# Kernel tuning notes

Measured on AMD Instinct MI355X. Metric: run time of the kernel, lower is better.

## Reference

```python
import jax, jax.numpy as jnp
import numpy as np

N, F, H = 512, 256, 512

def _w(k, i, o):
    return jax.random.normal(k, (i, o), jnp.float32) * (1.0 / np.sqrt(i))

def setup_inputs() -> dict:
    key = jax.random.key(0)
    ks = jax.random.split(key, 12)
    z = lambda n: jnp.zeros((n,), jnp.float32)
    return {
        "node_features": jax.random.normal(ks[0], (N, F), jnp.float32),
        "adjacency": jax.random.uniform(ks[1], (N, N), jnp.float32),
        # GraphConv layers: neighbor linear (wl,bl) and self-loop (ws,bs)
        "gc1_wl": _w(ks[2], F, H), "gc1_bl": z(H), "gc1_ws": _w(ks[3], F, H), "gc1_bs": z(H),
        "gc2_wl": _w(ks[4], H, H), "gc2_bl": z(H), "gc2_ws": _w(ks[5], H, H), "gc2_bs": z(H),
        "gc3_wl": _w(ks[6], H, F), "gc3_bl": z(F), "gc3_ws": _w(ks[7], H, F), "gc3_bs": z(F),
        # edge MLP: Linear(2F,H) -> ReLU -> (dropout=identity, eval) -> Linear(H,H) -> ReLU -> Linear(H,1)
        "mlp_w1": _w(ks[8], 2 * F, H), "mlp_b1": z(H),
        "mlp_w2": _w(ks[9], H, H), "mlp_b2": z(H),
        "mlp_w3": _w(ks[10], H, 1), "mlp_b3": z(1),
    }

def _gconv(x, adj_norm, wl, bl, ws, bs):
    # adj_norm @ Linear(x) + SelfLoop(x)
    return adj_norm @ (x @ wl + bl) + (x @ ws + bs)

def reference(node_features, adjacency,
              gc1_wl, gc1_bl, gc1_ws, gc1_bs,
              gc2_wl, gc2_bl, gc2_ws, gc2_bs,
              gc3_wl, gc3_bl, gc3_ws, gc3_bs,
              mlp_w1, mlp_b1, mlp_w2, mlp_b2, mlp_w3, mlp_b3):
    # row-normalized adjacency (shared across all three layers)
    adj_norm = adjacency / (adjacency.sum(axis=1, keepdims=True) + 1e-8)
    x = jax.nn.relu(_gconv(node_features, adj_norm, gc1_wl, gc1_bl, gc1_ws, gc1_bs))
    x = jax.nn.relu(_gconv(x, adj_norm, gc2_wl, gc2_bl, gc2_ws, gc2_bs))
    emb = _gconv(x, adj_norm, gc3_wl, gc3_bl, gc3_ws, gc3_bs)  # [N, F]
    # vectorized all-pairs (i<j) edge scoring, symmetric scatter
    iu, ju = np.triu_indices(N, k=1)  # static index lists, P = N(N-1)/2
    ef = jnp.concatenate([emb[iu], emb[ju]], axis=-1)  # [P, 2F]
    h = jax.nn.relu(ef @ mlp_w1 + mlp_b1)
    h = jax.nn.relu(h @ mlp_w2 + mlp_b2)
    s = jax.nn.sigmoid((h @ mlp_w3 + mlp_b3)[:, 0])  # [P]
    edge_scores = jnp.zeros((N, N), emb.dtype).at[iu, ju].set(s).at[ju, iu].set(s)
    return emb, edge_scores
```

## Files before the change

### kernel.cpp

```cpp
#include <hip/hip_runtime.h>
#include <hip/hip_bf16.h>


#define NN 512
#define FF 256
#define HH 512

typedef __attribute__((ext_vector_type(8))) short s8v;
typedef __attribute__((ext_vector_type(4))) float f4v;

__device__ __forceinline__ ushort f2bf(float f) {
  unsigned u = __float_as_uint(f);
  unsigned r = (u + 0x7fffu + ((u >> 16) & 1u)) >> 16;
  return (ushort)r;
}

template <bool RELU>
__device__ __forceinline__ void gemm_tile64(
    int m0, int n0, int K,
    const float* __restrict__ A, int lda,
    const float* __restrict__ B, int ldb,
    const float* __restrict__ bias,
    const float* __restrict__ add, int ldadd,
    float* __restrict__ C, int ldc, int tid)
{
  __shared__ float As[64][18];
  __shared__ float Bs[64][68];
  float4 acc = {0.f, 0.f, 0.f, 0.f};
  const int ty = tid >> 4, tx = tid & 15;

  const int am = tid >> 4;
  const int ak = tid & 15;
  const int bk = tid >> 4;
  const int bn = tid & 15;

  float4 pa = *(const float4*)&A[(m0 + am) * lda + ak * 4];
  float4 pb0 = *(const float4*)&B[bk * ldb + n0 + bn * 4];
  float4 pb1 = *(const float4*)&B[(bk + 16) * ldb + n0 + bn * 4];
  float4 pb2 = *(const float4*)&B[(bk + 32) * ldb + n0 + bn * 4];
  float4 pb3 = *(const float4*)&B[(bk + 48) * ldb + n0 + bn * 4];

  for (int k0 = 0; k0 < K; k0 += 64) {
    As[ak * 4 + 0][am] = pa.x;
    As[ak * 4 + 1][am] = pa.y;
    As[ak * 4 + 2][am] = pa.z;
    As[ak * 4 + 3][am] = pa.w;
    *(float4*)&Bs[bk][bn * 4] = pb0;
    *(float4*)&Bs[bk + 16][bn * 4] = pb1;
    *(float4*)&Bs[bk + 32][bn * 4] = pb2;
    *(float4*)&Bs[bk + 48][bn * 4] = pb3;
    __syncthreads();
    if (k0 + 64 < K) {
      pa = *(const float4*)&A[(m0 + am) * lda + k0 + 64 + ak * 4];
      pb0 = *(const float4*)&B[(k0 + 64 + bk) * ldb + n0 + bn * 4];
      pb1 = *(const float4*)&B[(k0 + 80 + bk) * ldb + n0 + bn * 4];
      pb2 = *(const float4*)&B[(k0 + 96 + bk) * ldb + n0 + bn * 4];
      pb3 = *(const float4*)&B[(k0 + 112 + bk) * ldb + n0 + bn * 4];
    }
#pragma unroll
    for (int k = 0; k < 64; ++k) {
      float a = As[k][ty];
      float4 b = *(const float4*)&Bs[k][tx * 4];
      acc.x += a * b.x; acc.y += a * b.y; acc.z += a * b.z; acc.w += a * b.w;
    }
    __syncthreads();
  }

  int m = m0 + ty;
  float4 v = acc;
  if (bias) {
    float4 bv = *(const float4*)&bias[n0 + tx * 4];
    v.x += bv.x; v.y += bv.y; v.z += bv.z; v.w += bv.w;
  }
  if (add) {
    float4 d = *(const float4*)&add[m * ldadd + n0 + tx * 4];
    v.x += d.x; v.y += d.y; v.z += d.z; v.w += d.w;
  }
  if (RELU) {
    v.x = fmaxf(v.x, 0.f); v.y = fmaxf(v.y, 0.f);
    v.z = fmaxf(v.z, 0.f); v.w = fmaxf(v.w, 0.f);
  }
  *(float4*)&C[m * ldc + n0 + tx * 4] = v;
}

template <bool RELU>
__global__ __launch_bounds__(512)
void gemm_ks(int K,
             const float* __restrict__ A, int lda,
             const float* __restrict__ B0, const float* __restrict__ B1, int ldb,
             const float* __restrict__ bias0, const float* __restrict__ bias1,
             const float* __restrict__ add0, const float* __restrict__ add1, int ldadd,
             float* __restrict__ C0, float* __restrict__ C1, int ldc)
{
  const float* B = blockIdx.z ? B1 : B0;
  const float* bias = blockIdx.z ? bias1 : bias0;
  const float* add = blockIdx.z ? add1 : add0;
  float* C = blockIdx.z ? C1 : C0;
  const int n0 = blockIdx.x * 64;
  const int m0 = blockIdx.y * 16;
  const int tid = threadIdx.x;
  const int half = tid >> 8;
  const int t = tid & 255;
  const int ty = t >> 4, tx = t & 15;

  __shared__ float As[2][64][18];
  __shared__ float Bs[2][64][68];
  __shared__ float red[16][68];

  float4 acc = {0.f, 0.f, 0.f, 0.f};
  const int am = t >> 4, ak = t & 15;
  const int bk = t >> 4, bn = t & 15;
  const int Kh = K >> 1;
  const int kb = half * Kh;

  float4 pa = *(const float4*)&A[(m0 + am) * lda + kb + ak * 4];
  float4 pb0 = *(const float4*)&B[(kb + bk) * ldb + n0 + bn * 4];
  float4 pb1 = *(const float4*)&B[(kb + bk + 16) * ldb + n0 + bn * 4];
  float4 pb2 = *(const float4*)&B[(kb + bk + 32) * ldb + n0 + bn * 4];
  float4 pb3 = *(const float4*)&B[(kb + bk + 48) * ldb + n0 + bn * 4];

  for (int k0 = 0; k0 < Kh; k0 += 64) {
    As[half][ak * 4 + 0][am] = pa.x;
    As[half][ak * 4 + 1][am] = pa.y;
    As[half][ak * 4 + 2][am] = pa.z;
    As[half][ak * 4 + 3][am] = pa.w;
    *(float4*)&Bs[half][bk][bn * 4] = pb0;
    *(float4*)&Bs[half][bk + 16][bn * 4] = pb1;
    *(float4*)&Bs[half][bk + 32][bn * 4] = pb2;
    *(float4*)&Bs[half][bk + 48][bn * 4] = pb3;
    __syncthreads();
    if (k0 + 64 < Kh) {
      pa = *(const float4*)&A[(m0 + am) * lda + kb + k0 + 64 + ak * 4];
      pb0 = *(const float4*)&B[(kb + k0 + 64 + bk) * ldb + n0 + bn * 4];
      pb1 = *(const float4*)&B[(kb + k0 + 80 + bk) * ldb + n0 + bn * 4];
      pb2 = *(const float4*)&B[(kb + k0 + 96 + bk) * ldb + n0 + bn * 4];
      pb3 = *(const float4*)&B[(kb + k0 + 112 + bk) * ldb + n0 + bn * 4];
    }
#pragma unroll
    for (int k = 0; k < 64; ++k) {
      float a = As[half][k][ty];
      float4 b = *(const float4*)&Bs[half][k][tx * 4];
      acc.x += a * b.x; acc.y += a * b.y; acc.z += a * b.z; acc.w += a * b.w;
    }
    __syncthreads();
  }

  if (half) *(float4*)&red[ty][tx * 4] = acc;
  __syncthreads();
  if (!half) {
    float4 r = *(const float4*)&red[ty][tx * 4];
    float4 v = acc;
    v.x += r.x; v.y += r.y; v.z += r.z; v.w += r.w;
    int m = m0 + ty;
    if (bias) {
      float4 bv = *(const float4*)&bias[n0 + tx * 4];
      v.x += bv.x; v.y += bv.y; v.z += bv.z; v.w += bv.w;
    }
    if (add) {
      float4 d = *(const float4*)&add[m * ldadd + n0 + tx * 4];
      v.x += d.x; v.y += d.y; v.z += d.z; v.w += d.w;
    }
    if (RELU) {
      v.x = fmaxf(v.x, 0.f); v.y = fmaxf(v.y, 0.f);
      v.z = fmaxf(v.z, 0.f); v.w = fmaxf(v.w, 0.f);
    }
    *(float4*)&C[m * ldc + n0 + tx * 4] = v;
  }
}

template <bool RELU>
__global__ __launch_bounds__(1024)
void gemm_ks4(int K,
              const float* __restrict__ A, int lda,
              const float* __restrict__ B0, const float* __restrict__ B1, int ldb,
              const float* __restrict__ bias0, const float* __restrict__ bias1,
              const float* __restrict__ add0, const float* __restrict__ add1, int ldadd,
              float* __restrict__ C0, float* __restrict__ C1, int ldc)
{
  const float* B = blockIdx.z ? B1 : B0;
  const float* bias = blockIdx.z ? bias1 : bias0;
  const float* add = blockIdx.z ? add1 : add0;
  float* C = blockIdx.z ? C1 : C0;
  const int n0 = blockIdx.x * 64;
  const int m0 = blockIdx.y * 16;
  const int tid = threadIdx.x;
  const int q = tid >> 8;
  const int t = tid & 255;
  const int ty = t >> 4, tx = t & 15;

  __shared__ float As[4][64][18];
  __shared__ float Bs[4][64][68];
  __shared__ float red[3][16][68];

  float4 acc = {0.f, 0.f, 0.f, 0.f};
  const int am = ty, ak = tx;
  const int bk = ty, bn = tx;
  const int Kq = K >> 2;
  const int kb = q * Kq;

  float4 pa = *(const float4*)&A[(m0 + am) * lda + kb + ak * 4];
  float4 pb0 = *(const float4*)&B[(kb + bk) * ldb + n0 + bn * 4];
  float4 pb1 = *(const float4*)&B[(kb + bk + 16) * ldb + n0 + bn * 4];
  float4 pb2 = *(const float4*)&B[(kb + bk + 32) * ldb + n0 + bn * 4];
  float4 pb3 = *(const float4*)&B[(kb + bk + 48) * ldb + n0 + bn * 4];

  for (int k0 = 0; k0 < Kq; k0 += 64) {
    As[q][ak * 4 + 0][am] = pa.x;
    As[q][ak * 4 + 1][am] = pa.y;
    As[q][ak * 4 + 2][am] = pa.z;
    As[q][ak * 4 + 3][am] = pa.w;
    *(float4*)&Bs[q][bk][bn * 4] = pb0;
    *(float4*)&Bs[q][bk + 16][bn * 4] = pb1;
    *(float4*)&Bs[q][bk + 32][bn * 4] = pb2;
    *(float4*)&Bs[q][bk + 48][bn * 4] = pb3;
    __syncthreads();
    if (k0 + 64 < Kq) {
      pa = *(const float4*)&A[(m0 + am) * lda + kb + k0 + 64 + ak * 4];
      pb0 = *(const float4*)&B[(kb + k0 + 64 + bk) * ldb + n0 + bn * 4];
      pb1 = *(const float4*)&B[(kb + k0 + 80 + bk) * ldb + n0 + bn * 4];
      pb2 = *(const float4*)&B[(kb + k0 + 96 + bk) * ldb + n0 + bn * 4];
      pb3 = *(const float4*)&B[(kb + k0 + 112 + bk) * ldb + n0 + bn * 4];
    }
#pragma unroll
    for (int k = 0; k < 64; ++k) {
      float a = As[q][k][ty];
      float4 b = *(const float4*)&Bs[q][k][tx * 4];
      acc.x += a * b.x; acc.y += a * b.y; acc.z += a * b.z; acc.w += a * b.w;
    }
    __syncthreads();
  }

  if (q) *(float4*)&red[q - 1][ty][tx * 4] = acc;
  __syncthreads();
  if (!q) {
    float4 v = acc;
#pragma unroll
    for (int r = 0; r < 3; ++r) {
      float4 p = *(const float4*)&red[r][ty][tx * 4];
      v.x += p.x; v.y += p.y; v.z += p.z; v.w += p.w;
    }
    int m = m0 + ty;
    if (bias) {
      float4 bv = *(const float4*)&bias[n0 + tx * 4];
      v.x += bv.x; v.y += bv.y; v.z += bv.z; v.w += bv.w;
    }
    if (add) {
      float4 d = *(const float4*)&add[m * ldadd + n0 + tx * 4];
      v.x += d.x; v.y += d.y; v.z += d.z; v.w += d.w;
    }
    if (RELU) {
      v.x = fmaxf(v.x, 0.f); v.y = fmaxf(v.y, 0.f);
      v.z = fmaxf(v.z, 0.f); v.w = fmaxf(v.w, 0.f);
    }
    *(float4*)&C[m * ldc + n0 + tx * 4] = v;
  }
}

__global__ __launch_bounds__(256)
void prep_gemm1(const float* __restrict__ adj, float* __restrict__ adjn,
                const float* __restrict__ w2, ushort* __restrict__ w2t2,
                const float* __restrict__ node,
                const float* __restrict__ g1wl, const float* __restrict__ g1bl,
                const float* __restrict__ g1ws, const float* __restrict__ g1bs,
                float* __restrict__ Tb, float* __restrict__ Sb) {
  int b = blockIdx.x;
  int tid = threadIdx.x;
  if (b < 512) {
    int z = b >> 8, t = b & 255;
    int m0 = (t >> 3) * 16, n0 = (t & 7) * 64;
    gemm_tile64<false>(m0, n0, FF, node, FF, z ? g1ws : g1wl, HH,
                       z ? g1bs : g1bl, nullptr, 0, z ? Sb : Tb, HH, tid);
  } else if (b < 1024) {
    int row = b - 512;
    const float* r = adj + row * NN;
    float a0 = r[tid], a1 = r[tid + 256];
    float s = a0 + a1;
#pragma unroll
    for (int m = 1; m < 64; m <<= 1) s += __shfl_xor(s, m);
    __shared__ float wsum[4];
    if ((tid & 63) == 0) wsum[tid >> 6] = s;
    __syncthreads();
    float inv = 1.f / (wsum[0] + wsum[1] + wsum[2] + wsum[3] + 1e-8f);
    float* o = adjn + row * NN;
    o[tid] = a0 * inv;
    o[tid + 256] = a1 * inv;
  } else {
    int b2 = b - 1024;
    int slab = b2 >> 3;
    int col = (b2 & 7) * 64 + (tid >> 2);
    int kq = tid & 3;
    int k0 = slab * 32 + kq * 8;
    ushort tmp[8];
#pragma unroll
    for (int e = 0; e < 8; ++e) tmp[e] = f2bf(w2[(k0 + e) * HH + col]);
    ushort* dst = w2t2 + slab * 16384 + col * 32 + kq * 8;
    *(ushort4*)dst = *(ushort4*)tmp;
    *(ushort4*)(dst + 4) = *(ushort4*)&tmp[4];
  }
}

__global__ __launch_bounds__(512)
__attribute__((amdgpu_waves_per_eu(2, 2)))
void edge_mlp(const float* __restrict__ Amat, const float* __restrict__ Bmat,
              const ushort* __restrict__ w2t2,
              const float* __restrict__ b2, const float* __restrict__ w3,
              const float* __restrict__ b3,
              float* __restrict__ edges)
{
  __shared__ ushort h1s[2][128 * 128];
  __shared__ float rowsv[2][24][128];
  __shared__ float part[8][128];

  const int tb = (int)blockIdx.x;
  int bj = (int)((sqrtf(4.f * tb + 1.f) - 1.f) * 0.5f);
  while (bj * bj + bj > tb) --bj;
  while ((bj + 1) * (bj + 2) <= tb) ++bj;
  const int bi = tb - bj * bj - bj;

  const int tid = threadIdx.x;
  const int wid = tid >> 6;
  const int lane = tid & 63;
  const int l15 = lane & 15;
  const int lg = lane >> 4;

  const f4v zero = {0.f, 0.f, 0.f, 0.f};
  f4v acc[8][4];
#pragma unroll
  for (int mf = 0; mf < 8; ++mf)
#pragma unroll
    for (int nf = 0; nf < 4; ++nf) acc[mf][nf] = zero;

  const int r1 = tid >> 5, kc1 = tid & 31;
  const int r2 = 16 + (tid >> 5);
  const float* src1base = (r1 < 8) ? (Amat + (bi * 8 + r1) * HH)
                                   : (Bmat + (bj * 16 + r1 - 8) * HH);
  const float* src2base = Bmat + (bj * 16 + r2 - 8) * HH;

  float4 ra, rb;
  auto issue_rows = [&](int ch) {
    ra = *(const float4*)(src1base + ch * 128 + kc1 * 4);
    if (tid < 256) rb = *(const float4*)(src2base + ch * 128 + kc1 * 4);
  };
  auto write_rows = [&](int buf) {
    *(float4*)&rowsv[buf][r1][kc1 * 4] = ra;
    if (tid < 256) *(float4*)&rowsv[buf][r2][kc1 * 4] = rb;
  };
  auto build_h1 = [&](int buf) {
#pragma unroll
    for (int q = 0; q < 8; ++q) {
      int fidx = q * 512 + tid;
      int p = fidx >> 5;
      int k4 = fidx & 31;
      float4 av = *(const float4*)&rowsv[buf][p >> 4][k4 * 4];
      float4 bv = *(const float4*)&rowsv[buf][8 + (p & 15)][k4 * 4];
      ushort4 pk;
      pk.x = f2bf(fmaxf(av.x + bv.x, 0.f));
      pk.y = f2bf(fmaxf(av.y + bv.y, 0.f));
      pk.z = f2bf(fmaxf(av.z + bv.z, 0.f));
      pk.w = f2bf(fmaxf(av.w + bv.w, 0.f));
      int off = (p * 256 + k4 * 8) ^ ((p & 7) << 4);
      *(ushort4*)((char*)h1s[buf] + off) = pk;
    }
  };

  auto lgkm_barrier = [] {
    asm volatile("s_waitcnt lgkmcnt(0)" ::: "memory");
    __builtin_amdgcn_s_barrier();
  };

  issue_rows(0);
  write_rows(0);
  lgkm_barrier();
  build_h1(0);
  lgkm_barrier();

  const ushort* wbase = w2t2 + wid * 2048 + l15 * 32 + lg * 8;

  s8v nb0, nb1, nb2, nb3;
  nb0 = *(const s8v*)wbase;
  nb1 = *(const s8v*)(wbase + 512);
  nb2 = *(const s8v*)(wbase + 1024);
  nb3 = *(const s8v*)(wbase + 1536);

  auto slab_step = [&](int cur, int slab) {
    s8v cb0 = nb0, cb1 = nb1, cb2 = nb2, cb3 = nb3;
    if (slab < 15) {
      const ushort* wb = wbase + (slab + 1) * 16384;
      nb0 = *(const s8v*)wb;
      nb1 = *(const s8v*)(wb + 512);
      nb2 = *(const s8v*)(wb + 1024);
      nb3 = *(const s8v*)(wb + 1536);
    }
    int ks = slab & 3;
    __builtin_amdgcn_s_setprio(1);
#pragma unroll
    for (int mf = 0; mf < 8; ++mf) {
      int p = mf * 16 + l15;
      int off = (p * 256 + ks * 64 + lg * 16) ^ ((p & 7) << 4);
      s8v a = *(const s8v*)((const char*)h1s[cur] + off);
      acc[mf][0] = __builtin_amdgcn_mfma_f32_16x16x32_bf16(a, cb0, acc[mf][0], 0, 0, 0);
      acc[mf][1] = __builtin_amdgcn_mfma_f32_16x16x32_bf16(a, cb1, acc[mf][1], 0, 0, 0);
      acc[mf][2] = __builtin_amdgcn_mfma_f32_16x16x32_bf16(a, cb2, acc[mf][2], 0, 0, 0);
      acc[mf][3] = __builtin_amdgcn_mfma_f32_16x16x32_bf16(a, cb3, acc[mf][3], 0, 0, 0);
    }
    __builtin_amdgcn_s_setprio(0);
  };

#pragma unroll
  for (int ch = 0; ch < 4; ++ch) {
    int cur = ch & 1;
    if (ch < 3) issue_rows(ch + 1);
    slab_step(cur, ch * 4 + 0);
    slab_step(cur, ch * 4 + 1);
    if (ch < 3) write_rows(cur ^ 1);
    slab_step(cur, ch * 4 + 2);
    if (ch < 3) lgkm_barrier();
    slab_step(cur, ch * 4 + 3);
    if (ch < 3) {
      build_h1(cur ^ 1);
      lgkm_barrier();
    }
  }

  float bb[4], ww[4];
#pragma unroll
  for (int nf = 0; nf < 4; ++nf) {
    int col = wid * 64 + nf * 16 + l15;
    bb[nf] = b2[col];
    ww[nf] = w3[col];
  }
#pragma unroll
  for (int mf = 0; mf < 8; ++mf) {
    float ps[4];
#pragma unroll
    for (int e = 0; e < 4; ++e) {
      ps[e] = fmaxf(acc[mf][0][e] + bb[0], 0.f) * ww[0] +
              fmaxf(acc[mf][1][e] + bb[1], 0.f) * ww[1] +
              fmaxf(acc[mf][2][e] + bb[2], 0.f) * ww[2] +
              fmaxf(acc[mf][3][e] + bb[3], 0.f) * ww[3];
    }
#pragma unroll
    for (int m = 1; m < 16; m <<= 1) {
#pragma unroll
      for (int e = 0; e < 4; ++e) ps[e] += __shfl_xor(ps[e], m);
    }
    if (l15 == 0) {
#pragma unroll
      for (int e = 0; e < 4; ++e)
        part[wid][mf * 16 + lg * 4 + e] = ps[e];
    }
  }
  __syncthreads();
  if (tid < 128) {
    float tot = b3[0];
#pragma unroll
    for (int w = 0; w < 8; ++w) tot += part[w][tid];
    float sg = 1.f / (1.f + expf(-tot));
    int i = bi * 8 + (tid >> 4);
    int j = bj * 16 + (tid & 15);
    if (i < j) {
      edges[i * NN + j] = sg;
      edges[j * NN + i] = sg;
    } else if (i == j) {
      edges[i * NN + i] = 0.f;
    }
  }
}

extern "C" void kernel_launch(void* const* d_in, const int* in_sizes, int n_in,
                              void* d_out, int out_size, void* d_ws, size_t ws_size,
                              hipStream_t stream) {
  const float* node = (const float*)d_in[0];
  const float* adj  = (const float*)d_in[1];
  const float* g1wl = (const float*)d_in[2];
  const float* g1bl = (const float*)d_in[3];
  const float* g1ws = (const float*)d_in[4];
  const float* g1bs = (const float*)d_in[5];
  const float* g2wl = (const float*)d_in[6];
  const float* g2bl = (const float*)d_in[7];
  const float* g2ws = (const float*)d_in[8];
  const float* g2bs = (const float*)d_in[9];
  const float* g3wl = (const float*)d_in[10];
  const float* g3bl = (const float*)d_in[11];
  const float* g3ws = (const float*)d_in[12];
  const float* g3bs = (const float*)d_in[13];
  const float* w1 = (const float*)d_in[14];
  const float* b1 = (const float*)d_in[15];
  const float* w2 = (const float*)d_in[16];
  const float* b2 = (const float*)d_in[17];
  const float* w3 = (const float*)d_in[18];
  const float* b3 = (const float*)d_in[19];

  float* out = (float*)d_out;
  float* emb = out;
  float* edges = out + NN * FF;

  char* wsb = (char*)d_ws;
  float* adjn = (float*)wsb;
  float* Tb   = (float*)(wsb + (1u << 20));
  float* Sb   = (float*)(wsb + (2u << 20));
  float* xa   = (float*)(wsb + (3u << 20));
  float* xb   = (float*)(wsb + (4u << 20));
  ushort* w2t2 = (ushort*)(wsb + (5u << 20));
  float* Amat = Tb;
  float* Bmat = Sb;

  prep_gemm1<<<1152, 256, 0, stream>>>(adj, adjn, w2, w2t2, node,
                                       g1wl, g1bl, g1ws, g1bs, Tb, Sb);
  gemm_ks4<true><<<dim3(8, 32, 1), 1024, 0, stream>>>(
      NN, adjn, NN, Tb, Tb, HH, nullptr, nullptr,
      Sb, Sb, HH, xa, xa, HH);
  gemm_ks<false><<<dim3(8, 32, 2), 512, 0, stream>>>(
      HH, xa, HH, g2wl, g2ws, HH, g2bl, g2bs,
      nullptr, nullptr, 0, Tb, Sb, HH);
  gemm_ks4<true><<<dim3(8, 32, 1), 1024, 0, stream>>>(
      NN, adjn, NN, Tb, Tb, HH, nullptr, nullptr,
      Sb, Sb, HH, xb, xb, HH);
  gemm_ks4<false><<<dim3(4, 32, 2), 1024, 0, stream>>>(
      HH, xb, HH, g3wl, g3ws, FF, g3bl, g3bs,
      nullptr, nullptr, 0, Tb, Sb, FF);
  gemm_ks4<false><<<dim3(4, 32, 1), 1024, 0, stream>>>(
      NN, adjn, NN, Tb, Tb, FF, nullptr, nullptr,
      Sb, Sb, FF, emb, emb, FF);
  gemm_ks<false><<<dim3(8, 32, 2), 512, 0, stream>>>(
      FF, emb, FF, w1, w1 + FF * HH, HH, b1, nullptr,
      nullptr, nullptr, 0, Amat, Bmat, HH);

  edge_mlp<<<1056, 512, 0, stream>>>(Amat, Bmat, w2t2, b2, w3, b3, edges);
}
```

Baseline: 166.7 us.

## Reassociate layer-3 and first MLP linear via precomposed weights, cutting a dependent GEMM

Layer 3 is restructured as V3 = adjn @ xb, then emb and the MLP's first-layer projections Amat/Bmat are all computed directly from [V3, xb] against precomposed weight products (g3wl@w1 etc.) built in the prep kernel. This removes one serial GEMM from the dependency chain and merges the remaining ones into a single concatenated-K launch. The cost is extra weight-product GEMMs in prep, a bias-fold loop, more workspace, and changed fp32 rounding order. The path is gated on workspace size.

```diff
diff --git a/kernel.cpp b/kernel.cpp
--- a/kernel.cpp
+++ b/kernel.cpp
@@ -256,13 +256,100 @@
   }
 }
 
+__global__ __launch_bounds__(512)
+void gemm_cat(const float* __restrict__ V3, const float* __restrict__ xb,
+              const float* __restrict__ g3wl, const float* __restrict__ g3ws,
+              const float* __restrict__ CwA1, const float* __restrict__ CwA2,
+              const float* __restrict__ CwB1, const float* __restrict__ CwB2,
+              const float* __restrict__ g3b, const float* __restrict__ biasA,
+              const float* __restrict__ biasB,
+              float* __restrict__ emb, float* __restrict__ Amat,
+              float* __restrict__ Bmat)
+{
+  const int z = blockIdx.z;
+  if (z == 0 && blockIdx.x >= 4) return;
+  const float* B1; const float* B2; const float* bias; float* C;
+  int ldb, ldc;
+  if (z == 0)      { B1 = g3wl; B2 = g3ws; bias = g3b;   C = emb;  ldb = 256; ldc = 256; }
+  else if (z == 1) { B1 = CwA1; B2 = CwA2; bias = biasA; C = Amat; ldb = 512; ldc = 512; }
+  else             { B1 = CwB1; B2 = CwB2; bias = biasB; C = Bmat; ldb = 512; ldc = 512; }
+
+  const int n0 = blockIdx.x * 64;
+  const int m0 = blockIdx.y * 16;
+  const int tid = threadIdx.x;
+  const int half = tid >> 8;
+  const int t = tid & 255;
+  const int ty = t >> 4, tx = t & 15;
+  const float* A = half ? xb : V3;
+  const float* B = half ? B2 : B1;
+
+  __shared__ float As[2][64][18];
+  __shared__ float Bs[2][64][68];
+  __shared__ float red[16][68];
+
+  float4 acc = {0.f, 0.f, 0.f, 0.f};
+  const int am = ty, ak = tx;
+  const int bk = ty, bn = tx;
+
+  float4 pa = *(const float4*)&A[(m0 + am) * 512 + ak * 4];
+  float4 pb0 = *(const float4*)&B[bk * ldb + n0 + bn * 4];
+  float4 pb1 = *(const float4*)&B[(bk + 16) * ldb + n0 + bn * 4];
+  float4 pb2 = *(const float4*)&B[(bk + 32) * ldb + n0 + bn * 4];
+  float4 pb3 = *(const float4*)&B[(bk + 48) * ldb + n0 + bn * 4];
+
+  for (int k0 = 0; k0 < 512; k0 += 64) {
+    As[half][ak * 4 + 0][am] = pa.x;
+    As[half][ak * 4 + 1][am] = pa.y;
+    As[half][ak * 4 + 2][am] = pa.z;
+    As[half][ak * 4 + 3][am] = pa.w;
+    *(float4*)&Bs[half][bk][bn * 4] = pb0;
+    *(float4*)&Bs[half][bk + 16][bn * 4] = pb1;
+    *(float4*)&Bs[half][bk + 32][bn * 4] = pb2;
+    *(float4*)&Bs[half][bk + 48][bn * 4] = pb3;
+    __syncthreads();
+    if (k0 + 64 < 512) {
+      pa = *(const float4*)&A[(m0 + am) * 512 + k0 + 64 + ak * 4];
+      pb0 = *(const float4*)&B[(k0 + 64 + bk) * ldb + n0 + bn * 4];
+      pb1 = *(const float4*)&B[(k0 + 80 + bk) * ldb + n0 + bn * 4];
+      pb2 = *(const float4*)&B[(k0 + 96 + bk) * ldb + n0 + bn * 4];
+      pb3 = *(const float4*)&B[(k0 + 112 + bk) * ldb + n0 + bn * 4];
+    }
+#pragma unroll
+    for (int k = 0; k < 64; ++k) {
+      float a = As[half][k][ty];
+      float4 b = *(const float4*)&Bs[half][k][tx * 4];
+      acc.x += a * b.x; acc.y += a * b.y; acc.z += a * b.z; acc.w += a * b.w;
+    }
+    __syncthreads();
+  }
+
+  if (half) *(float4*)&red[ty][tx * 4] = acc;
+  __syncthreads();
+  if (!half) {
+    float4 r = *(const float4*)&red[ty][tx * 4];
+    float4 v = acc;
+    v.x += r.x; v.y += r.y; v.z += r.z; v.w += r.w;
+    float4 bv = *(const float4*)&bias[n0 + tx * 4];
+    v.x += bv.x; v.y += bv.y; v.z += bv.z; v.w += bv.w;
+    *(float4*)&C[(m0 + ty) * ldc + n0 + tx * 4] = v;
+  }
+}
+
 __global__ __launch_bounds__(256)
 void prep_gemm1(const float* __restrict__ adj, float* __restrict__ adjn,
                 const float* __restrict__ w2, ushort* __restrict__ w2t2,
                 const float* __restrict__ node,
                 const float* __restrict__ g1wl, const float* __restrict__ g1bl,
                 const float* __restrict__ g1ws, const float* __restrict__ g1bs,
-                float* __restrict__ Tb, float* __restrict__ Sb) {
+                float* __restrict__ Tb, float* __restrict__ Sb,
+                int do_fused,
+                const float* __restrict__ g3wl, const float* __restrict__ g3ws,
+                const float* __restrict__ g3bl, const float* __restrict__ g3bs,
+                const float* __restrict__ w1, const float* __restrict__ b1,
+                float* __restrict__ CwA1, float* __restrict__ CwA2,
+                float* __restrict__ CwB1, float* __restrict__ CwB2,
+                float* __restrict__ g3b, float* __restrict__ biasA,
+                float* __restrict__ biasB) {
   int b = blockIdx.x;
   int tid = threadIdx.x;
   if (b < 512) {
@@ -284,7 +371,7 @@
     float* o = adjn + row * NN;
     o[tid] = a0 * inv;
     o[tid + 256] = a1 * inv;
-  } else {
+  } else if (b < 1152) {
     int b2 = b - 1024;
     int slab = b2 >> 3;
     int col = (b2 & 7) * 64 + (tid >> 2);
@@ -296,6 +383,34 @@
     ushort* dst = w2t2 + slab * 16384 + col * 32 + kq * 8;
     *(ushort4*)dst = *(ushort4*)tmp;
     *(ushort4*)(dst + 4) = *(ushort4*)&tmp[4];
+  } else if (b < 2176) {
+    if (!do_fused) return;
+    int c = (b - 1152) >> 8;
+    int t = (b - 1152) & 255;
+    int m0 = (t >> 3) * 16, n0 = (t & 7) * 64;
+    const float* A = (c & 1) ? g3ws : g3wl;
+    const float* B = w1 + ((c >> 1) ? FF * HH : 0);
+    float* C = (c == 0) ? CwA1 : (c == 1) ? CwA2 : (c == 2) ? CwB1 : CwB2;
+    gemm_tile64<false>(m0, n0, FF, A, FF, B, HH, nullptr, nullptr, 0,
+                       C, HH, tid);
+  } else {
+    if (!do_fused) return;
+    __shared__ float gb[256];
+    gb[tid] = g3bl[tid] + g3bs[tid];
+    g3b[tid] = gb[tid];
+    __syncthreads();
+#pragma unroll
+    for (int rep = 0; rep < 2; ++rep) {
+      int n = tid + rep * 256;
+      float sa = b1[n], sb = 0.f;
+      for (int f = 0; f < 256; ++f) {
+        float g = gb[f];
+        sa += g * w1[f * HH + n];
+        sb += g * w1[(FF + f) * HH + n];
+      }
+      biasA[n] = sa;
+      biasB[n] = sb;
+    }
   }
 }
 
@@ -502,11 +617,23 @@
   float* xa   = (float*)(wsb + (3u << 20));
   float* xb   = (float*)(wsb + (4u << 20));
   ushort* w2t2 = (ushort*)(wsb + (5u << 20));
+  float* CwA1 = (float*)(wsb + (5u << 20) + (512u << 10));
+  float* CwA2 = (float*)(wsb + (6u << 20) + (512u << 10));
+  float* CwB1 = (float*)(wsb + (7u << 20) + (512u << 10));
+  float* CwB2 = (float*)(wsb + (8u << 20) + (512u << 10));
+  float* g3b  = (float*)(wsb + (9u << 20) + (512u << 10));
+  float* biasA = g3b + 1024;
+  float* biasB = biasA + 512;
   float* Amat = Tb;
   float* Bmat = Sb;
-
-  prep_gemm1<<<1152, 256, 0, stream>>>(adj, adjn, w2, w2t2, node,
-                                       g1wl, g1bl, g1ws, g1bs, Tb, Sb);
+  float* V3 = xa;
+
+  const int fused = (ws_size >= (10u << 20)) ? 1 : 0;
+
+  prep_gemm1<<<fused ? 2177 : 1152, 256, 0, stream>>>(
+      adj, adjn, w2, w2t2, node, g1wl, g1bl, g1ws, g1bs, Tb, Sb,
+      fused, g3wl, g3ws, g3bl, g3bs, w1, b1,
+      CwA1, CwA2, CwB1, CwB2, g3b, biasA, biasB);
   gemm_ks4<true><<<dim3(8, 32, 1), 1024, 0, stream>>>(
       NN, adjn, NN, Tb, Tb, HH, nullptr, nullptr,
       Sb, Sb, HH, xa, xa, HH);
@@ -516,15 +643,25 @@
   gemm_ks4<true><<<dim3(8, 32, 1), 1024, 0, stream>>>(
       NN, adjn, NN, Tb, Tb, HH, nullptr, nullptr,
       Sb, Sb, HH, xb, xb, HH);
-  gemm_ks4<false><<<dim3(4, 32, 2), 1024, 0, stream>>>(
-      HH, xb, HH, g3wl, g3ws, FF, g3bl, g3bs,
-      nullptr, nullptr, 0, Tb, Sb, FF);
-  gemm_ks4<false><<<dim3(4, 32, 1), 1024, 0, stream>>>(
-      NN, adjn, NN, Tb, Tb, FF, nullptr, nullptr,
-      Sb, Sb, FF, emb, emb, FF);
-  gemm_ks<false><<<dim3(8, 32, 2), 512, 0, stream>>>(
-      FF, emb, FF, w1, w1 + FF * HH, HH, b1, nullptr,
-      nullptr, nullptr, 0, Amat, Bmat, HH);
+
+  if (fused) {
+    gemm_ks<false><<<dim3(8, 32, 1), 512, 0, stream>>>(
+        NN, adjn, NN, xb, xb, HH, nullptr, nullptr,
+        nullptr, nullptr, 0, V3, V3, HH);
+    gemm_cat<<<dim3(8, 32, 3), 512, 0, stream>>>(
+        V3, xb, g3wl, g3ws, CwA1, CwA2, CwB1, CwB2,
+        g3b, biasA, biasB, emb, Amat, Bmat);
+  } else {
+    gemm_ks4<false><<<dim3(4, 32, 2), 1024, 0, stream>>>(
+        HH, xb, HH, g3wl, g3ws, FF, g3bl, g3bs,
+        nullptr, nullptr, 0, Tb, Sb, FF);
+    gemm_ks4<false><<<dim3(4, 32, 1), 1024, 0, stream>>>(
+        NN, adjn, NN, Tb, Tb, FF, nullptr, nullptr,
+        Sb, Sb, FF, emb, emb, FF);
+    gemm_ks<false><<<dim3(8, 32, 2), 512, 0, stream>>>(
+        FF, emb, FF, w1, w1 + FF * HH, HH, b1, nullptr,
+        nullptr, nullptr, 0, Amat, Bmat, HH);
+  }
 
   edge_mlp<<<1056, 512, 0, stream>>>(Amat, Bmat, w2t2, b2, w3, b3, edges);
 }
```

After: 223.8 us. 34.2% more time.
